# Performance work log

Hardware: AMD Instinct MI355X
Metric: run time of the kernel (lower is better)

Reference implementation:

```python
import jax, jax.numpy as jnp
import numpy as np
from jax import lax

EPS = 1e-5
D_STATE = 16
D_CONV = 4
DT_RANK = 4  # ceil(d_model/16) with d_model=64 (mamba_ssm default)


def _conv3d(x, w, pad, groups=1):
    return lax.conv_general_dilated(
        x, w, (1, 1, 1), pad,
        dimension_numbers=('NCDHW', 'OIDHW', 'NCDHW'),
        feature_group_count=groups)


def _inorm(x, g, b):
    # InstanceNorm3d: per-sample, per-channel stats over (Z,H,W), biased var, eps=1e-5
    m = x.mean(axis=(2, 3, 4), keepdims=True)
    v = x.var(axis=(2, 3, 4), keepdims=True)
    xn = (x - m) * lax.rsqrt(v + EPS)
    return xn * g[None, :, None, None, None] + b[None, :, None, None, None]


def _ln(x, g, b):
    m = x.mean(-1, keepdims=True)
    v = x.var(-1, keepdims=True)
    return (x - m) * lax.rsqrt(v + EPS) * g + b


def _forward(x, c1_w, in1_g, in1_b, c2_w, in2_g, in2_b,
             dw_w, pw_w, inr_g, inr_b,
             ln_g, ln_b,
             in_proj_w, conv1d_w, conv1d_b, x_proj_w,
             dt_proj_w, dt_proj_b, A_log, D_p, out_proj_w,
             proj_w, proj_b, pn_g, pn_b):
    B, _, Z, H, W = x.shape
    pad233 = [(1, 1), (1, 1), (1, 1)]  # kernel (2,3,3): Z grows by 1 each conv
    # ---- VolumeConvBlock ----
    h = _conv3d(x, c1_w, pad233)
    h = jax.nn.leaky_relu(_inorm(h, in1_g, in1_b), 0.01)
    h = _conv3d(h, c2_w, pad233)
    h = jax.nn.leaky_relu(_inorm(h, in2_g, in2_b), 0.01)
    h = h[:, :, :Z]  # out[:, :, :x.shape[2]]
    C = h.shape[1]
    # ---- ZMambaBlock ----
    residual = h
    # DepthwiseSpatialRefine
    pre = _conv3d(h, dw_w, [(0, 0), (1, 1), (1, 1)], groups=C)
    pre = _conv3d(pre, pw_w, [(0, 0), (0, 0), (0, 0)])
    pre = jax.nn.silu(_inorm(pre, inr_g, inr_b))
    x2 = h + pre
    # [B,C,Z,H,W] -> [B*H*W, Z, C]
    seq = jnp.transpose(x2, (0, 3, 4, 2, 1)).reshape(B * H * W, Z, C)
    seq = _ln(seq, ln_g, ln_b)
    # ---- Mamba ----
    di = in_proj_w.shape[0] // 2  # d_inner
    xz = seq @ in_proj_w.T  # [N, Z, 2*di]
    x_in, z = xz[..., :di], xz[..., di:]
    # causal depthwise conv1d along Z (pad left d_conv-1 == pad both then truncate)
    xc = lax.conv_general_dilated(
        jnp.transpose(x_in, (0, 2, 1)), conv1d_w, (1,), [(D_CONV - 1, 0)],
        dimension_numbers=('NCH', 'OIH', 'NCH'), feature_group_count=di)
    xc = xc + conv1d_b[None, :, None]
    xa = jax.nn.silu(jnp.transpose(xc, (0, 2, 1)))  # [N, Z, di]
    x_dbl = xa @ x_proj_w.T  # [N, Z, dt_rank + 2*d_state]
    dt = jax.nn.softplus(x_dbl[..., :DT_RANK] @ dt_proj_w.T + dt_proj_b)  # [N,Z,di]
    Bm = x_dbl[..., DT_RANK:DT_RANK + D_STATE]  # [N,Z,ds]
    Cm = x_dbl[..., DT_RANK + D_STATE:]         # [N,Z,ds]
    A = -jnp.exp(A_log)  # [di, ds]
    N = xa.shape[0]

    def step(hst, inp):
        dt_t, B_t, C_t, u_t = inp  # [N,di],[N,ds],[N,ds],[N,di]
        hst = jnp.exp(dt_t[:, :, None] * A) * hst + (dt_t * u_t)[:, :, None] * B_t[:, None, :]
        y_t = jnp.einsum('nds,ns->nd', hst, C_t)
        return hst, y_t

    h0 = jnp.zeros((N, di, D_STATE), dtype=xa.dtype)
    _, ys = lax.scan(step, h0,
                     (jnp.transpose(dt, (1, 0, 2)), jnp.transpose(Bm, (1, 0, 2)),
                      jnp.transpose(Cm, (1, 0, 2)), jnp.transpose(xa, (1, 0, 2))))
    y = jnp.transpose(ys, (1, 0, 2)) + D_p * xa  # [N,Z,di]
    y = y * jax.nn.silu(z)
    seq = y @ out_proj_w.T  # back to [N,Z,C]
    # proj linear
    seq = seq @ proj_w.T + proj_b
    # [B*H*W,Z,C] -> [B,C,Z,H,W]
    x3 = jnp.transpose(seq.reshape(B, H, W, Z, C), (0, 4, 3, 1, 2))
    x3 = _inorm(x3, pn_g, pn_b)
    return residual + x3


def setup_inputs() -> dict:
    key = jax.random.key(0)
    ks = jax.random.split(key, 20)
    IC, OC = 32, 64
    DI = 2 * OC  # d_inner = expand * d_model
    B, Z, H, W = 1, 32, 64, 64
    f32 = jnp.float32
    inp = {
        'x': jax.random.normal(ks[0], (B, IC, Z, H, W), f32),
        'c1_w': jax.random.normal(ks[1], (OC, IC, 2, 3, 3), f32) * 0.05,
        'in1_g': jnp.ones((OC,), f32), 'in1_b': jnp.zeros((OC,), f32),
        'c2_w': jax.random.normal(ks[2], (OC, OC, 2, 3, 3), f32) * 0.04,
        'in2_g': jnp.ones((OC,), f32), 'in2_b': jnp.zeros((OC,), f32),
        'dw_w': jax.random.normal(ks[3], (OC, 1, 1, 3, 3), f32) * 0.3,
        'pw_w': jax.random.normal(ks[4], (OC, OC, 1, 1, 1), f32) * 0.12,
        'inr_g': jnp.ones((OC,), f32), 'inr_b': jnp.zeros((OC,), f32),
        'ln_g': jnp.ones((OC,), f32), 'ln_b': jnp.zeros((OC,), f32),
        'in_proj_w': jax.random.normal(ks[5], (2 * DI, OC), f32) * 0.12,
        'conv1d_w': jax.random.normal(ks[6], (DI, 1, D_CONV), f32) * 0.4,
        'conv1d_b': jnp.zeros((DI,), f32),
        'x_proj_w': jax.random.normal(ks[7], (DT_RANK + 2 * D_STATE, DI), f32) * 0.08,
        'dt_proj_w': jax.random.normal(ks[8], (DI, DT_RANK), f32) * 0.4,
        'dt_proj_b': jax.random.uniform(ks[9], (DI,), f32, -4.0, -1.0),
        'A_log': jnp.log(jnp.tile(jnp.arange(1, D_STATE + 1, dtype=f32), (DI, 1))),
        'D_p': jnp.ones((DI,), f32),
        'out_proj_w': jax.random.normal(ks[10], (OC, DI), f32) * 0.08,
        'proj_w': jax.random.normal(ks[11], (OC, OC), f32) * 0.12,
        'proj_b': jnp.zeros((OC,), f32),
        'pn_g': jnp.ones((OC,), f32), 'pn_b': jnp.zeros((OC,), f32),
    }
    return inp


def reference(x, c1_w, in1_g, in1_b, c2_w, in2_g, in2_b,
              dw_w, pw_w, inr_g, inr_b, ln_g, ln_b,
              in_proj_w, conv1d_w, conv1d_b, x_proj_w,
              dt_proj_w, dt_proj_b, A_log, D_p, out_proj_w,
              proj_w, proj_b, pn_g, pn_b):
    return _forward(x, c1_w, in1_g, in1_b, c2_w, in2_g, in2_b,
                    dw_w, pw_w, inr_g, inr_b, ln_g, ln_b,
                    in_proj_w, conv1d_w, conv1d_b, x_proj_w,
                    dt_proj_w, dt_proj_b, A_log, D_p, out_proj_w,
                    proj_w, proj_b, pn_g, pn_b)
```

## Files before the change

kernel.cpp:

```cpp
#include <hip/hip_runtime.h>
#include <hip/hip_bf16.h>

#define NTHREADS 256

typedef __attribute__((ext_vector_type(8))) short bs8_t;
typedef __attribute__((ext_vector_type(4))) float f4_t;

__device__ __forceinline__ float bf2f(__hip_bfloat16 v) { return __bfloat162float(v); }
__device__ __forceinline__ __hip_bfloat16 f2bf(float v) { return __float2bfloat16(v); }
__device__ __forceinline__ float b2f_lo(unsigned int p) { return __uint_as_float(p << 16); }
__device__ __forceinline__ float b2f_hi(unsigned int p) { return __uint_as_float(p & 0xffff0000u); }
__device__ __forceinline__ float sigm(float x) { return 1.f / (1.f + __expf(-x)); }
__device__ __forceinline__ float leaky(float x) { return x > 0.f ? x : 0.01f * x; }
__device__ __forceinline__ float sane(float x) { return fminf(fmaxf(x, -1e9f), 1e9f); }
__device__ __forceinline__ unsigned packbf(float a, float b) {
  union { __hip_bfloat16 h[2]; unsigned u; } cv;
  cv.h[0] = f2bf(a); cv.h[1] = f2bf(b);
  return cv.u;
}
__device__ __forceinline__ float ldf(const void* p, long i, int f) {
  return f ? ((const float*)p)[i] : bf2f(((const __hip_bfloat16*)p)[i]);
}
__device__ __forceinline__ float exp2_fast(float x) {
  float r;
  asm("v_exp_f32 %0, %1" : "=v"(r) : "v"(x));
  return r;
}

__global__ void k_detect(const void* xp, int* flag) {
  __shared__ int cnt[NTHREADS];
  const __hip_bfloat16* h = (const __hip_bfloat16*)xp;
  int t = threadIdx.x;
  int c = 0;
  for (int j = 0; j < 8; j++) {
    float v = fabsf(bf2f(h[(t * 8 + j) * 2]));
    if (v > 1e-12f && v < 1e12f) c++;
  }
  cnt[t] = c;
  __syncthreads();
  for (int s = 128; s > 0; s >>= 1) {
    if (t < s) cnt[t] += cnt[t + s];
    __syncthreads();
  }
  if (t == 0) *flag = (cnt[0] > 1433) ? 0 : 1;
}

__global__ void k_prepcvt(const void* __restrict__ in, __hip_bfloat16* __restrict__ out,
                          int n, const int* __restrict__ flagp) {
  int f = *flagp;
  int gid = blockIdx.x * NTHREADS + threadIdx.x;
  if (gid < n) out[gid] = f2bf(ldf(in, gid, f));
}

__global__ __launch_bounds__(NTHREADS) void k_pad1(const void* __restrict__ x,
                                                   __hip_bfloat16* __restrict__ P1,
                                                   const int* __restrict__ flagp) {
  __shared__ float tile[64 * 33];
  int f = *flagp;
  int zp = blockIdx.x / 66, yp = blockIdx.x % 66;
  long rowbase = ((long)zp * 66 + yp) * 66 * 32;
  int t = threadIdx.x;
  if (zp == 0 || zp == 33 || yp == 0 || yp == 65) {
    for (int i = t; i < 2112; i += NTHREADS) P1[rowbase + i] = f2bf(0.f);
    return;
  }
  int z = zp - 1, y = yp - 1;
#pragma unroll
  for (int j = 0; j < 8; j++) {
    int idx = t + j * NTHREADS;
    int ci = idx >> 6, xx = idx & 63;
    tile[xx * 33 + ci] = ldf(x, (long)(ci * 32 + z) * 4096 + y * 64 + xx, f);
  }
  __syncthreads();
#pragma unroll
  for (int j = 0; j < 8; j++) {
    int idx = t + j * NTHREADS;
    int xx = idx >> 5, ci = idx & 31;
    P1[rowbase + (xx + 1) * 32 + ci] = f2bf(tile[xx * 33 + ci]);
  }
  if (t < 32) P1[rowbase + t] = f2bf(0.f);
  else if (t < 64) P1[rowbase + 65 * 32 + (t - 32)] = f2bf(0.f);
}

__global__ void k_prepw(const void* __restrict__ cw, __hip_bfloat16* __restrict__ W,
                        int CI, const int* __restrict__ flagp) {
  int f = *flagp;
  int gid = blockIdx.x * NTHREADS + threadIdx.x;
  int s = gid / (64 * CI);
  int rem = gid % (64 * CI);
  int co = rem / CI, ci = rem % CI;
  W[gid] = f2bf(ldf(cw, (long)(co * CI + ci) * 18 + s, f));
}

template <int CI, int CIP>
__global__ __launch_bounds__(NTHREADS) void k_gemm_conv(const __hip_bfloat16* __restrict__ Pb,
                                                        const __hip_bfloat16* __restrict__ Wb,
                                                        __hip_bfloat16* __restrict__ out,
                                                        float* __restrict__ gacc) {
  __shared__ unsigned short Wl[3 * 64 * CIP];
  __shared__ float sred[256], qred[256];
  const unsigned short* P = (const unsigned short*)Pb;
  const unsigned short* W = (const unsigned short*)Wb;
  int t = threadIdx.x;
  int wv = t >> 6, lane = t & 63;
  int m = lane & 15, quad = lane >> 4;
  int zo  = blockIdx.x >> 5;
  int rem = blockIdx.x & 31;
  int y   = ((rem >> 1) << 2) + wv;
  int xb  = (rem & 1) << 5;
  f4_t zero4 = {0.f, 0.f, 0.f, 0.f};
  f4_t acc[2][4];
#pragma unroll
  for (int mt = 0; mt < 2; mt++)
#pragma unroll
    for (int nt = 0; nt < 4; nt++) acc[mt][nt] = zero4;

  const int NV = 3 * 64 * CI / 8;
  for (int kz = 0; kz < 2; kz++) {
    for (int ky = 0; ky < 3; ky++) {
      __syncthreads();
      int s0 = (kz * 3 + ky) * 3;
      const uint4* wsrc4 = (const uint4*)(W + (long)s0 * 64 * CI);
      for (int i4 = t; i4 < NV; i4 += NTHREADS) {
        int idx = i4 * 8;
        int kx = idx / (64 * CI), rem2 = idx % (64 * CI);
        int co = rem2 / CI, g = (rem2 % CI) >> 3;
        *(uint4*)&Wl[(kx * 64 + co) * CIP + g * 8] = wsrc4[i4];
      }
      __syncthreads();
      int pz = zo + kz, py = y + ky;
      const unsigned short* prow = P + ((long)(pz * 66 + py) * 66) * CI;
#pragma unroll
      for (int kx = 0; kx < 3; kx++) {
#pragma unroll
        for (int ch = 0; ch < CI / 32; ch++) {
          int kof = kx * CI + ch * 32 + quad * 8;
          bs8_t a0 = *(const bs8_t*)(prow + (xb + 0 * 16 + m) * CI + kof);
          bs8_t a1 = *(const bs8_t*)(prow + (xb + 1 * 16 + m) * CI + kof);
#pragma unroll
          for (int nt = 0; nt < 4; nt++) {
            bs8_t b = *(const bs8_t*)&Wl[(kx * 64 + nt * 16 + m) * CIP + ch * 32 + quad * 8];
            acc[0][nt] = __builtin_amdgcn_mfma_f32_16x16x32_bf16(a0, b, acc[0][nt], 0, 0, 0);
            acc[1][nt] = __builtin_amdgcn_mfma_f32_16x16x32_bf16(a1, b, acc[1][nt], 0, 0, 0);
          }
        }
      }
    }
  }
  long obase = ((long)(zo * 64 + y) * 64) * 64;
  float psum[4], pq[4];
#pragma unroll
  for (int nt = 0; nt < 4; nt++) {
    int co = nt * 16 + m;
    float s = 0.f, q = 0.f;
#pragma unroll
    for (int mt = 0; mt < 2; mt++)
#pragma unroll
      for (int rg = 0; rg < 4; rg++) {
        float v = acc[mt][nt][rg];
        int xx = xb + mt * 16 + quad * 4 + rg;
        out[obase + xx * 64 + co] = f2bf(v);
        s += v;
        q += v * v;
      }
    psum[nt] = s;
    pq[nt] = q;
  }
#pragma unroll
  for (int nt = 0; nt < 4; nt++) {
    psum[nt] += __shfl_xor(psum[nt], 16, 64);
    psum[nt] += __shfl_xor(psum[nt], 32, 64);
    pq[nt]   += __shfl_xor(pq[nt], 16, 64);
    pq[nt]   += __shfl_xor(pq[nt], 32, 64);
  }
  if (quad == 0) {
#pragma unroll
    for (int nt = 0; nt < 4; nt++) {
      sred[wv * 64 + nt * 16 + m] = psum[nt];
      qred[wv * 64 + nt * 16 + m] = pq[nt];
    }
  }
  __syncthreads();
  if (t < 64) {
    atomicAdd(&gacc[t], sred[t] + sred[64 + t] + sred[128 + t] + sred[192 + t]);
    atomicAdd(&gacc[64 + t], qred[t] + qred[64 + t] + qred[128 + t] + qred[192 + t]);
  }
}

__global__ void k_finalize(const float* __restrict__ acc, const void* __restrict__ g,
                           const void* __restrict__ b, float* __restrict__ ss, float invN,
                           const int* __restrict__ flagp) {
  int f = *flagp;
  int t = threadIdx.x;
  float mean = acc[t] * invN;
  float var  = acc[64 + t] * invN - mean * mean;
  float rstd = rsqrtf(fmaxf(var, 0.f) + 1e-5f);
  float sc   = ldf(g, t, f) * rstd;
  ss[t]      = sc;
  ss[64 + t] = ldf(b, t, f) - mean * sc;
}

__global__ __launch_bounds__(NTHREADS) void k_normpad(const __hip_bfloat16* __restrict__ in,
                                                      const float* __restrict__ ss,
                                                      __hip_bfloat16* __restrict__ P2) {
  int zp = blockIdx.x / 66, yp = blockIdx.x % 66;
  long rowbase = ((long)zp * 66 + yp) * 66 * 64;
  int t = threadIdx.x;
  if (zp == 0 || zp == 34 || yp == 0 || yp == 65) {
    for (int i = t; i < 4224; i += NTHREADS) P2[rowbase + i] = f2bf(0.f);
    return;
  }
  int z = zp - 1, y = yp - 1;
#pragma unroll
  for (int j = 0; j < 16; j++) {
    int idx = t + j * NTHREADS;
    int xx = idx >> 6, co = idx & 63;
    float v = bf2f(in[((long)(z * 64 + y) * 64 + xx) * 64 + co]) * ss[co] + ss[64 + co];
    P2[rowbase + (xx + 1) * 64 + co] = f2bf(leaky(v));
  }
  if (t < 64) P2[rowbase + t] = f2bf(0.f);
  else if (t < 128) P2[rowbase + 65 * 64 + (t - 64)] = f2bf(0.f);
}

__global__ __launch_bounds__(NTHREADS) void k_hslice_cl(const __hip_bfloat16* __restrict__ in,
                                                        const float* __restrict__ ss,
                                                        __hip_bfloat16* __restrict__ hcl,
                                                        void* __restrict__ resid,
                                                        const int* __restrict__ flagp) {
  __shared__ float tile[64 * 65];
  int f = *flagp;
  int z = blockIdx.x >> 6, y = blockIdx.x & 63;
  long r0 = (long)z * 4096 + y * 64;
  int t = threadIdx.x;
#pragma unroll
  for (int j = 0; j < 16; j++) {
    int idx = t + j * NTHREADS;
    int xx = idx >> 6, co = idx & 63;
    float v = leaky(bf2f(in[(r0 + xx) * 64 + co]) * ss[co] + ss[64 + co]);
    hcl[(r0 + xx) * 64 + co] = f2bf(v);
    tile[xx * 65 + co] = v;
  }
  __syncthreads();
#pragma unroll
  for (int j = 0; j < 16; j++) {
    int idx = t + j * NTHREADS;
    int co = idx >> 6, xx = idx & 63;
    long off = (long)co * 131072 + r0 + xx;
    if (f) ((float*)resid)[off] = tile[xx * 65 + co];
    else   ((__hip_bfloat16*)resid)[off] = f2bf(tile[xx * 65 + co]);
  }
}

__global__ __launch_bounds__(NTHREADS) void k_dwpw_mfma(const __hip_bfloat16* __restrict__ hcl,
                                                        const void* __restrict__ dwb,
                                                        const __hip_bfloat16* __restrict__ pwbb,
                                                        __hip_bfloat16* __restrict__ out,
                                                        float* __restrict__ acc,
                                                        const int* __restrict__ flagp) {
  __shared__ unsigned short hl[3 * 64 * 64];
  __shared__ unsigned short dwt[64 * 72];
  __shared__ unsigned short pwl[64 * 72];
  __shared__ float dwl[576];
  __shared__ float sred[256], qred[256];
  int f = *flagp;
  int t = threadIdx.x;
  int z = blockIdx.x >> 6, y = blockIdx.x & 63;
  for (int i = t; i < 576; i += NTHREADS) dwl[i] = ldf(dwb, i, f);
  {
    const uint4* ps4 = (const uint4*)pwbb;
#pragma unroll
    for (int j = 0; j < 2; j++) {
      int i = t + j * NTHREADS;
      int row = i >> 3, g = i & 7;
      *(uint4*)&pwl[row * 72 + g * 8] = ps4[i];
    }
  }
  {
    const unsigned short* hsrc = (const unsigned short*)hcl;
    uint4* hl4 = (uint4*)hl;
#pragma unroll
    for (int j = 0; j < 6; j++) {
      int i = t + j * NTHREADS;
      int dy = i / 512, rem = i % 512;
      int ry = y - 1 + dy;
      uint4 v = make_uint4(0u, 0u, 0u, 0u);
      if ((unsigned)ry < 64u)
        v = *(const uint4*)(hsrc + ((long)z * 4096 + ry * 64) * 64 + rem * 8);
      hl4[i] = v;
    }
  }
  __syncthreads();
  const unsigned* hl32 = (const unsigned*)hl;
  unsigned* dwt32 = (unsigned*)dwt;
#pragma unroll
  for (int j = 0; j < 8; j++) {
    int idx = t + j * NTHREADS;
    int xx = idx >> 5, cp = idx & 31;
    float a0 = 0.f, a1 = 0.f;
#pragma unroll
    for (int dy = 0; dy < 3; dy++)
#pragma unroll
      for (int dx = 0; dx < 3; dx++) {
        int xv = xx - 1 + dx;
        if ((unsigned)xv < 64u) {
          unsigned hv = hl32[(dy * 64 + xv) * 32 + cp];
          a0 = fmaf(b2f_lo(hv), dwl[(cp * 2) * 9 + dy * 3 + dx], a0);
          a1 = fmaf(b2f_hi(hv), dwl[(cp * 2 + 1) * 9 + dy * 3 + dx], a1);
        }
      }
    dwt32[xx * 36 + cp] = packbf(a0, a1);
  }
  __syncthreads();
  int wv = t >> 6, lane = t & 63;
  int m = lane & 15, quad = lane >> 4;
  f4_t zero4 = {0.f, 0.f, 0.f, 0.f};
  f4_t acc4[4];
#pragma unroll
  for (int nt = 0; nt < 4; nt++) acc4[nt] = zero4;
#pragma unroll
  for (int ch = 0; ch < 2; ch++) {
    bs8_t a = *(const bs8_t*)&dwt[(wv * 16 + m) * 72 + ch * 32 + quad * 8];
#pragma unroll
    for (int nt = 0; nt < 4; nt++) {
      bs8_t b = *(const bs8_t*)&pwl[(nt * 16 + m) * 72 + ch * 32 + quad * 8];
      acc4[nt] = __builtin_amdgcn_mfma_f32_16x16x32_bf16(a, b, acc4[nt], 0, 0, 0);
    }
  }
  long obase = ((long)z * 4096 + y * 64) * 64;
  float psum[4], pq[4];
#pragma unroll
  for (int nt = 0; nt < 4; nt++) {
    float s = 0.f, q = 0.f;
#pragma unroll
    for (int rg = 0; rg < 4; rg++) {
      float v = acc4[nt][rg];
      int xx = wv * 16 + quad * 4 + rg;
      out[obase + xx * 64 + nt * 16 + m] = f2bf(v);
      s += v;
      q += v * v;
    }
    psum[nt] = s;
    pq[nt] = q;
  }
#pragma unroll
  for (int nt = 0; nt < 4; nt++) {
    psum[nt] += __shfl_xor(psum[nt], 16, 64);
    psum[nt] += __shfl_xor(psum[nt], 32, 64);
    pq[nt]   += __shfl_xor(pq[nt], 16, 64);
    pq[nt]   += __shfl_xor(pq[nt], 32, 64);
  }
  if (quad == 0) {
#pragma unroll
    for (int nt = 0; nt < 4; nt++) {
      sred[wv * 64 + nt * 16 + m] = psum[nt];
      qred[wv * 64 + nt * 16 + m] = pq[nt];
    }
  }
  __syncthreads();
  if (t < 64) {
    atomicAdd(&acc[t], sred[t] + sred[64 + t] + sred[128 + t] + sred[192 + t]);
    atomicAdd(&acc[64 + t], qred[t] + qred[64 + t] + qred[128 + t] + qred[192 + t]);
  }
}

__global__ __launch_bounds__(NTHREADS) void k_x2ln_cl(const __hip_bfloat16* __restrict__ hcl,
                                                      const __hip_bfloat16* __restrict__ p2,
                                                      const float* __restrict__ ssr,
                                                      const void* __restrict__ lng,
                                                      const void* __restrict__ lnb,
                                                      __hip_bfloat16* __restrict__ out,
                                                      const int* __restrict__ flagp) {
  __shared__ float sc[64], sh[64], sg[64], sb[64];
  int f = *flagp;
  int t = threadIdx.x;
  if (t < 64) {
    sc[t] = ssr[t];
    sh[t] = ssr[64 + t];
    sg[t] = ldf(lng, t, f);
    sb[t] = ldf(lnb, t, f);
  }
  __syncthreads();
  long r = (long)blockIdx.x * NTHREADS + t;
  const uint4* hp = (const uint4*)(hcl + r * 64);
  const uint4* pp = (const uint4*)(p2 + r * 64);
  float v[64];
  float s1 = 0.f;
#pragma unroll
  for (int q = 0; q < 8; q++) {
    uint4 hu = hp[q], pu = pp[q];
    float hv[8] = {b2f_lo(hu.x), b2f_hi(hu.x), b2f_lo(hu.y), b2f_hi(hu.y),
                   b2f_lo(hu.z), b2f_hi(hu.z), b2f_lo(hu.w), b2f_hi(hu.w)};
    float pv[8] = {b2f_lo(pu.x), b2f_hi(pu.x), b2f_lo(pu.y), b2f_hi(pu.y),
                   b2f_lo(pu.z), b2f_hi(pu.z), b2f_lo(pu.w), b2f_hi(pu.w)};
#pragma unroll
    for (int i = 0; i < 8; i++) {
      int c = q * 8 + i;
      float pn = sc[c] * pv[i] + sh[c];
      float x2 = hv[i] + pn * sigm(pn);
      v[c] = x2;
      s1 += x2;
    }
  }
  float m = s1 * (1.f / 64.f);
  float s2 = 0.f;
#pragma unroll
  for (int c = 0; c < 64; c++) {
    float d = v[c] - m;
    s2 += d * d;
  }
  float rstd = rsqrtf(s2 * (1.f / 64.f) + 1e-5f);
  uint4* o4 = (uint4*)(out + r * 64);
#pragma unroll
  for (int q = 0; q < 8; q++) {
    int c = q * 8;
    uint4 o;
    o.x = packbf((v[c + 0] - m) * rstd * sg[c + 0] + sb[c + 0],
                 (v[c + 1] - m) * rstd * sg[c + 1] + sb[c + 1]);
    o.y = packbf((v[c + 2] - m) * rstd * sg[c + 2] + sb[c + 2],
                 (v[c + 3] - m) * rstd * sg[c + 3] + sb[c + 3]);
    o.z = packbf((v[c + 4] - m) * rstd * sg[c + 4] + sb[c + 4],
                 (v[c + 5] - m) * rstd * sg[c + 5] + sb[c + 5]);
    o.w = packbf((v[c + 6] - m) * rstd * sg[c + 6] + sb[c + 6],
                 (v[c + 7] - m) * rstd * sg[c + 7] + sb[c + 7]);
    o4[q] = o;
  }
}

__global__ __launch_bounds__(NTHREADS) void k_inproj_mfma(const __hip_bfloat16* __restrict__ seq,
                                                          const __hip_bfloat16* __restrict__ Wbf,
                                                          __hip_bfloat16* __restrict__ x_in,
                                                          __hip_bfloat16* __restrict__ zg) {
  __shared__ unsigned short Wl[256 * 72];
  const uint4* ws4 = (const uint4*)Wbf;
  int t = threadIdx.x;
#pragma unroll
  for (int j = 0; j < 8; j++) {
    int i4 = t + j * NTHREADS;
    int row = i4 >> 3, g = i4 & 7;
    *(uint4*)&Wl[row * 72 + g * 8] = ws4[i4];
  }
  __syncthreads();
  int wv = t >> 6, lane = t & 63;
  int m = lane & 15, quad = lane >> 4;
  long m0 = (long)blockIdx.x * 64;
  int n0 = wv * 64;
  f4_t zero4 = {0.f, 0.f, 0.f, 0.f};
  f4_t acc[4][4];
#pragma unroll
  for (int mt = 0; mt < 4; mt++)
#pragma unroll
    for (int nt = 0; nt < 4; nt++) acc[mt][nt] = zero4;
  const unsigned short* sp = (const unsigned short*)seq;
#pragma unroll
  for (int ch = 0; ch < 2; ch++) {
    int kof = ch * 32 + quad * 8;
    bs8_t a0 = *(const bs8_t*)(sp + (m0 + 0 * 16 + m) * 64 + kof);
    bs8_t a1 = *(const bs8_t*)(sp + (m0 + 1 * 16 + m) * 64 + kof);
    bs8_t a2 = *(const bs8_t*)(sp + (m0 + 2 * 16 + m) * 64 + kof);
    bs8_t a3 = *(const bs8_t*)(sp + (m0 + 3 * 16 + m) * 64 + kof);
#pragma unroll
    for (int nt = 0; nt < 4; nt++) {
      bs8_t b = *(const bs8_t*)&Wl[(n0 + nt * 16 + m) * 72 + kof];
      acc[0][nt] = __builtin_amdgcn_mfma_f32_16x16x32_bf16(a0, b, acc[0][nt], 0, 0, 0);
      acc[1][nt] = __builtin_amdgcn_mfma_f32_16x16x32_bf16(a1, b, acc[1][nt], 0, 0, 0);
      acc[2][nt] = __builtin_amdgcn_mfma_f32_16x16x32_bf16(a2, b, acc[2][nt], 0, 0, 0);
      acc[3][nt] = __builtin_amdgcn_mfma_f32_16x16x32_bf16(a3, b, acc[3][nt], 0, 0, 0);
    }
  }
  __hip_bfloat16* obuf = (n0 < 128) ? x_in : zg;
  int cbase = (n0 < 128) ? n0 : (n0 - 128);
#pragma unroll
  for (int mt = 0; mt < 4; mt++)
#pragma unroll
    for (int nt = 0; nt < 4; nt++) {
      int col = cbase + nt * 16 + m;
#pragma unroll
      for (int rg = 0; rg < 4; rg++) {
        long row = m0 + mt * 16 + quad * 4 + rg;
        obuf[row * 128 + col] = f2bf(acc[mt][nt][rg]);
      }
    }
}

__global__ __launch_bounds__(NTHREADS) void k_conv1d_ip(__hip_bfloat16* xio,
                                                        const void* __restrict__ wb,
                                                        const void* __restrict__ bb,
                                                        const int* __restrict__ flagp) {
  int f = *flagp;
  int gid = blockIdx.x * NTHREADS + threadIdx.x;
  int d = gid & 127, nl = gid >> 7;
  float w0 = ldf(wb, d * 4 + 0, f), w1 = ldf(wb, d * 4 + 1, f);
  float w2 = ldf(wb, d * 4 + 2, f), w3 = ldf(wb, d * 4 + 3, f);
  float bias = ldf(bb, d, f);
  const size_t stride = 4096u * 128u;
  size_t off0 = (size_t)nl * 128 + d;
  float xv[32];
#pragma unroll
  for (int z = 0; z < 32; z++) xv[z] = bf2f(xio[off0 + (size_t)z * stride]);
  float h0 = 0.f, h1 = 0.f, h2 = 0.f;
#pragma unroll
  for (int z = 0; z < 32; z++) {
    float cur = xv[z];
    float a = bias;
    a = fmaf(h0, w0, a);
    a = fmaf(h1, w1, a);
    a = fmaf(h2, w2, a);
    a = fmaf(cur, w3, a);
    xv[z] = a * sigm(a);
    h0 = h1; h1 = h2; h2 = cur;
  }
#pragma unroll
  for (int z = 0; z < 32; z++) xio[off0 + (size_t)z * stride] = f2bf(xv[z]);
}

__global__ __launch_bounds__(NTHREADS) void k_xproj_mfma(const __hip_bfloat16* __restrict__ A,
                                                         const __hip_bfloat16* __restrict__ Wbf,
                                                         float* __restrict__ dtin,
                                                         float* __restrict__ BC) {
  __shared__ unsigned short Wl[48 * 136];
  const uint4* ws4 = (const uint4*)Wbf;
  int t = threadIdx.x;
#pragma unroll
  for (int j = 0; j < 3; j++) {
    int i4 = t + j * NTHREADS;
    int row = i4 >> 4, g = i4 & 15;
    uint4 v = make_uint4(0u, 0u, 0u, 0u);
    if (row < 36) v = ws4[row * 16 + g];
    *(uint4*)&Wl[row * 136 + g * 8] = v;
  }
  __syncthreads();
  int wv = t >> 6, lane = t & 63;
  int m = lane & 15, quad = lane >> 4;
  long m0 = (long)blockIdx.x * 256 + wv * 64;
  f4_t zero4 = {0.f, 0.f, 0.f, 0.f};
  f4_t acc[4][3];
#pragma unroll
  for (int mt = 0; mt < 4; mt++)
#pragma unroll
    for (int nt = 0; nt < 3; nt++) acc[mt][nt] = zero4;
  const unsigned short* ap = (const unsigned short*)A;
#pragma unroll
  for (int ch = 0; ch < 4; ch++) {
    int kof = ch * 32 + quad * 8;
    bs8_t a0 = *(const bs8_t*)(ap + (m0 + 0 * 16 + m) * 128 + kof);
    bs8_t a1 = *(const bs8_t*)(ap + (m0 + 1 * 16 + m) * 128 + kof);
    bs8_t a2 = *(const bs8_t*)(ap + (m0 + 2 * 16 + m) * 128 + kof);
    bs8_t a3 = *(const bs8_t*)(ap + (m0 + 3 * 16 + m) * 128 + kof);
#pragma unroll
    for (int nt = 0; nt < 3; nt++) {
      bs8_t b = *(const bs8_t*)&Wl[(nt * 16 + m) * 136 + kof];
      acc[0][nt] = __builtin_amdgcn_mfma_f32_16x16x32_bf16(a0, b, acc[0][nt], 0, 0, 0);
      acc[1][nt] = __builtin_amdgcn_mfma_f32_16x16x32_bf16(a1, b, acc[1][nt], 0, 0, 0);
      acc[2][nt] = __builtin_amdgcn_mfma_f32_16x16x32_bf16(a2, b, acc[2][nt], 0, 0, 0);
      acc[3][nt] = __builtin_amdgcn_mfma_f32_16x16x32_bf16(a3, b, acc[3][nt], 0, 0, 0);
    }
  }
#pragma unroll
  for (int mt = 0; mt < 4; mt++)
#pragma unroll
    for (int nt = 0; nt < 3; nt++) {
      int col = nt * 16 + m;
#pragma unroll
      for (int rg = 0; rg < 4; rg++) {
        long row = m0 + mt * 16 + quad * 4 + rg;
        float v = acc[mt][nt][rg];
        if (col < 4) dtin[row * 4 + col] = v;
        else if (col < 36) BC[row * 32 + (col - 4)] = v;
      }
    }
}

__global__ __launch_bounds__(NTHREADS) void k_scan(const float* __restrict__ dtin,
                                                   const float* __restrict__ BC,
                                                   __hip_bfloat16* __restrict__ uy,
                                                   const __hip_bfloat16* __restrict__ zg,
                                                   const void* __restrict__ dtw,
                                                   const void* __restrict__ dtb,
                                                   const void* __restrict__ Alog,
                                                   const void* __restrict__ Dp,
                                                   const int* __restrict__ flagp) {
  int f = *flagp;
  int gid = blockIdx.x * NTHREADS + threadIdx.x;
  int d = gid & 127, n = gid >> 7;
  float A2[16];
#pragma unroll
  for (int s = 0; s < 16; s++)
    A2[s] = -__expf(fminf(ldf(Alog, d * 16 + s, f), 60.f)) * 1.44269504088896f;
  float W0 = ldf(dtw, d * 4 + 0, f), W1 = ldf(dtw, d * 4 + 1, f);
  float W2 = ldf(dtw, d * 4 + 2, f), W3 = ldf(dtw, d * 4 + 3, f);
  float bias = ldf(dtb, d, f);
  float Dv = ldf(Dp, d, f);
  float a0 = A2[0];
  int geo = 1;
#pragma unroll
  for (int s = 1; s < 16; s++)
    geo &= (fabsf(A2[s] - (float)(s + 1) * a0) <= 1e-4f * fabsf(A2[s])) ? 1 : 0;
  geo = __all(geo);
  float st[16];
#pragma unroll
  for (int s = 0; s < 16; s++) st[s] = 0.f;
  if (geo) {
    int nu_ = __builtin_amdgcn_readfirstlane(n);
    const float4* bp0 = (const float4*)(BC + (size_t)nu_ * 32);
    const float4* dp0 = (const float4*)(dtin + (size_t)nu_ * 4);
    const __hip_bfloat16* up0 = uy + (size_t)n * 128 + d;
    const __hip_bfloat16* zp0 = zg + (size_t)n * 128 + d;
    __hip_bfloat16* uq = uy + (size_t)n * 128 + d;
    const size_t ustep = 4096u * 128u;
    float4 b0 = bp0[0], b1 = bp0[1], b2 = bp0[2], b3 = bp0[3];
    float4 c0 = bp0[4], c1 = bp0[5], c2 = bp0[6], c3 = bp0[7];
    float4 dt4 = dp0[0];
    float u  = sane(bf2f(*up0));
    float zv = sane(bf2f(*zp0));
#pragma unroll 2
    for (int z = 0; z < 32; z++) {
      int zn = (z < 31) ? z + 1 : 31;
      const float4* bpn = bp0 + (size_t)zn * 32768u;
      float4 nb0 = bpn[0], nb1 = bpn[1], nb2 = bpn[2], nb3 = bpn[3];
      float4 nc0 = bpn[4], nc1 = bpn[5], nc2 = bpn[6], nc3 = bpn[7];
      float4 ndt = dp0[(size_t)zn * 4096u];
      float nu  = sane(bf2f(up0[(size_t)zn * ustep]));
      float nzv = sane(bf2f(zp0[(size_t)zn * ustep]));
      float v = bias;
      v = fmaf(dt4.x, W0, v);
      v = fmaf(dt4.y, W1, v);
      v = fmaf(dt4.z, W2, v);
      v = fmaf(dt4.w, W3, v);
      float dtv = v > 20.f ? v : __logf(1.f + __expf(v));
      dtv = fminf(fmaxf(dtv, 0.f), 60.f);
      float du = dtv * u;
      float e1 = exp2_fast(dtv * a0);
      float e2 = e1 * e1;
      float es[16];
      es[0] = e1; es[1] = e2;
#pragma unroll
      for (int s = 2; s < 16; s++) es[s] = es[s - 2] * e2;
      float B[16] = {b0.x, b0.y, b0.z, b0.w, b1.x, b1.y, b1.z, b1.w,
                     b2.x, b2.y, b2.z, b2.w, b3.x, b3.y, b3.z, b3.w};
      float C[16] = {c0.x, c0.y, c0.z, c0.w, c1.x, c1.y, c1.z, c1.w,
                     c2.x, c2.y, c2.z, c2.w, c3.x, c3.y, c3.z, c3.w};
#pragma unroll
      for (int s = 0; s < 16; s++) st[s] = fmaf(es[s], st[s], du * B[s]);
      float y0 = 0.f, y1 = 0.f, y2 = 0.f, y3 = 0.f;
#pragma unroll
      for (int s = 0; s < 16; s += 4) {
        y0 = fmaf(st[s + 0], C[s + 0], y0);
        y1 = fmaf(st[s + 1], C[s + 1], y1);
        y2 = fmaf(st[s + 2], C[s + 2], y2);
        y3 = fmaf(st[s + 3], C[s + 3], y3);
      }
      float y = (y0 + y1) + (y2 + y3);
      y = sane((y + Dv * u) * (zv * sigm(zv)));
      uq[(size_t)z * ustep] = f2bf(y);
      b0 = nb0; b1 = nb1; b2 = nb2; b3 = nb3;
      c0 = nc0; c1 = nc1; c2 = nc2; c3 = nc3;
      dt4 = ndt; u = nu; zv = nzv;
    }
  } else {
#pragma unroll
    for (int s = 0; s < 16; s++) asm("" : "+v"(A2[s]));
    for (int z = 0; z < 32; z++) {
      size_t r = (size_t)z * 4096 + n;
      const float4* bp = (const float4*)(BC + r * 32);
      float4 dt4 = *(const float4*)(dtin + r * 4);
      float4 b0 = bp[0], b1 = bp[1], b2 = bp[2], b3 = bp[3];
      float4 c0 = bp[4], c1 = bp[5], c2 = bp[6], c3 = bp[7];
      float u = sane(bf2f(uy[r * 128 + d]));
      float zv = sane(bf2f(zg[r * 128 + d]));
      float v = bias;
      v = fmaf(dt4.x, W0, v);
      v = fmaf(dt4.y, W1, v);
      v = fmaf(dt4.z, W2, v);
      v = fmaf(dt4.w, W3, v);
      float dtv = v > 20.f ? v : __logf(1.f + __expf(v));
      dtv = fminf(fmaxf(dtv, 0.f), 60.f);
      float du = dtv * u;
      float B[16] = {b0.x, b0.y, b0.z, b0.w, b1.x, b1.y, b1.z, b1.w,
                     b2.x, b2.y, b2.z, b2.w, b3.x, b3.y, b3.z, b3.w};
      float C[16] = {c0.x, c0.y, c0.z, c0.w, c1.x, c1.y, c1.z, c1.w,
                     c2.x, c2.y, c2.z, c2.w, c3.x, c3.y, c3.z, c3.w};
      float y = 0.f;
#pragma unroll
      for (int s = 0; s < 16; s++) {
        float e = exp2_fast(dtv * A2[s]);
        st[s] = fmaf(e, st[s], du * B[s]);
        y = fmaf(st[s], C[s], y);
      }
      y = sane((y + Dv * u) * (zv * sigm(zv)));
      uy[r * 128 + d] = f2bf(y);
    }
  }
}

__global__ void k_wcomb(const void* __restrict__ pw, const void* __restrict__ opw,
                        __hip_bfloat16* __restrict__ wc, const int* __restrict__ flagp) {
  int f = *flagp;
  int gid = blockIdx.x * NTHREADS + threadIdx.x;
  int d = gid & 127, o = gid >> 7;
  float a = 0.f;
#pragma unroll
  for (int j = 0; j < 64; j++) a = fmaf(ldf(pw, o * 64 + j, f), ldf(opw, j * 128 + d, f), a);
  wc[(size_t)o * 128 + d] = f2bf(a);
}

__global__ __launch_bounds__(NTHREADS) void k_outproj_mfma(const __hip_bfloat16* __restrict__ A,
                                                           const __hip_bfloat16* __restrict__ Wcb,
                                                           const void* __restrict__ bias,
                                                           __hip_bfloat16* __restrict__ out,
                                                           float* __restrict__ gacc,
                                                           const int* __restrict__ flagp) {
  __shared__ unsigned short Wl[64 * 136];
  __shared__ float bl[64];
  __shared__ float sred[256], qred[256];
  int f = *flagp;
  int t = threadIdx.x;
  const uint4* ws4 = (const uint4*)Wcb;
#pragma unroll
  for (int j = 0; j < 4; j++) {
    int i4 = t + j * NTHREADS;
    int row = i4 >> 4, g = i4 & 15;
    *(uint4*)&Wl[row * 136 + g * 8] = ws4[i4];
  }
  if (t < 64) bl[t] = ldf(bias, t, f);
  __syncthreads();
  int wv = t >> 6, lane = t & 63;
  int m = lane & 15, quad = lane >> 4;
  long m0 = (long)blockIdx.x * 256 + wv * 64;
  f4_t zero4 = {0.f, 0.f, 0.f, 0.f};
  f4_t acc[4][4];
#pragma unroll
  for (int mt = 0; mt < 4; mt++)
#pragma unroll
    for (int nt = 0; nt < 4; nt++) acc[mt][nt] = zero4;
  const unsigned short* ap = (const unsigned short*)A;
#pragma unroll
  for (int ch = 0; ch < 4; ch++) {
    int kof = ch * 32 + quad * 8;
    bs8_t a0 = *(const bs8_t*)(ap + (m0 + 0 * 16 + m) * 128 + kof);
    bs8_t a1 = *(const bs8_t*)(ap + (m0 + 1 * 16 + m) * 128 + kof);
    bs8_t a2 = *(const bs8_t*)(ap + (m0 + 2 * 16 + m) * 128 + kof);
    bs8_t a3 = *(const bs8_t*)(ap + (m0 + 3 * 16 + m) * 128 + kof);
#pragma unroll
    for (int nt = 0; nt < 4; nt++) {
      bs8_t b = *(const bs8_t*)&Wl[(nt * 16 + m) * 136 + kof];
      acc[0][nt] = __builtin_amdgcn_mfma_f32_16x16x32_bf16(a0, b, acc[0][nt], 0, 0, 0);
      acc[1][nt] = __builtin_amdgcn_mfma_f32_16x16x32_bf16(a1, b, acc[1][nt], 0, 0, 0);
      acc[2][nt] = __builtin_amdgcn_mfma_f32_16x16x32_bf16(a2, b, acc[2][nt], 0, 0, 0);
      acc[3][nt] = __builtin_amdgcn_mfma_f32_16x16x32_bf16(a3, b, acc[3][nt], 0, 0, 0);
    }
  }
  float psum[4], pq[4];
#pragma unroll
  for (int nt = 0; nt < 4; nt++) {
    int co = nt * 16 + m;
    float s = 0.f, q = 0.f;
#pragma unroll
    for (int mt = 0; mt < 4; mt++)
#pragma unroll
      for (int rg = 0; rg < 4; rg++) {
        float v = sane(acc[mt][nt][rg] + bl[co]);
        long row = m0 + mt * 16 + quad * 4 + rg;
        out[row * 64 + co] = f2bf(v);
        s += v;
        q += v * v;
      }
    psum[nt] = s;
    pq[nt] = q;
  }
#pragma unroll
  for (int nt = 0; nt < 4; nt++) {
    psum[nt] += __shfl_xor(psum[nt], 16, 64);
    psum[nt] += __shfl_xor(psum[nt], 32, 64);
    pq[nt]   += __shfl_xor(pq[nt], 16, 64);
    pq[nt]   += __shfl_xor(pq[nt], 32, 64);
  }
  if (quad == 0) {
#pragma unroll
    for (int nt = 0; nt < 4; nt++) {
      sred[wv * 64 + nt * 16 + m] = psum[nt];
      qred[wv * 64 + nt * 16 + m] = pq[nt];
    }
  }
  __syncthreads();
  if (t < 64) {
    atomicAdd(&gacc[t], sred[t] + sred[64 + t] + sred[128 + t] + sred[192 + t]);
    atomicAdd(&gacc[64 + t], qred[t] + qred[64 + t] + qred[128 + t] + qred[192 + t]);
  }
}

__global__ __launch_bounds__(NTHREADS) void k_final(const __hip_bfloat16* __restrict__ s2,
                                                    void* __restrict__ io,
                                                    const float* __restrict__ ss,
                                                    const int* __restrict__ flagp) {
  __shared__ float tile[64 * 65];
  __shared__ float sc[64], sh[64];
  int f = *flagp;
  int t = threadIdx.x;
  if (t < 64) {
    sc[t] = ss[t];
    sh[t] = ss[64 + t];
  }
  int z = blockIdx.x >> 6, n0 = (blockIdx.x & 63) << 6;
  size_t base = ((size_t)z * 4096 + n0) * 64;
  __syncthreads();
#pragma unroll
  for (int jj = 0; jj < 16; jj++) {
    int id = t + jj * NTHREADS;
    int i = id >> 6, c = id & 63;
    float v = sane(bf2f(s2[base + id]));
    tile[i * 65 + c] = sc[c] * v + sh[c];
  }
  __syncthreads();
#pragma unroll
  for (int jj = 0; jj < 16; jj++) {
    int id = t + jj * NTHREADS;
    int c = id >> 6, nl = id & 63;
    size_t off = (size_t)c * 131072 + (size_t)z * 4096 + n0 + nl;
    if (f) {
      float* o = (float*)io;
      o[off] = sane(o[off] + tile[nl * 65 + c]);
    } else {
      __hip_bfloat16* o = (__hip_bfloat16*)io;
      o[off] = f2bf(sane(bf2f(o[off]) + tile[nl * 65 + c]));
    }
  }
}

extern "C" void kernel_launch(void* const* d_in, const int* in_sizes, int n_in,
                              void* d_out, int out_size, void* d_ws, size_t ws_size,
                              hipStream_t stream) {
  (void)in_sizes; (void)n_in; (void)out_size; (void)ws_size;
  const void* x        = d_in[0];
  const void* c1_w     = d_in[1];
  const void* in1_g    = d_in[2];
  const void* in1_b    = d_in[3];
  const void* c2_w     = d_in[4];
  const void* in2_g    = d_in[5];
  const void* in2_b    = d_in[6];
  const void* dw_w     = d_in[7];
  const void* pw_w     = d_in[8];
  const void* inr_g    = d_in[9];
  const void* inr_b    = d_in[10];
  const void* ln_g     = d_in[11];
  const void* ln_b     = d_in[12];
  const void* in_proj_w= d_in[13];
  const void* conv1d_w = d_in[14];
  const void* conv1d_b = d_in[15];
  const void* x_proj_w = d_in[16];
  const void* dt_proj_w= d_in[17];
  const void* dt_proj_b= d_in[18];
  const void* A_log    = d_in[19];
  const void* D_p      = d_in[20];
  const void* out_proj_w=d_in[21];
  const void* proj_w   = d_in[22];
  const void* proj_b   = d_in[23];
  const void* pn_g     = d_in[24];
  const void* pn_b     = d_in[25];

  char* wb = (char*)d_ws;
  __hip_bfloat16* P1   = (__hip_bfloat16*)wb;
  __hip_bfloat16* P2   = (__hip_bfloat16*)wb;
  __hip_bfloat16* zgb  = (__hip_bfloat16*)wb;
  __hip_bfloat16* s2   = (__hip_bfloat16*)wb;
  __hip_bfloat16* c1raw = (__hip_bfloat16*)(wb + 33554432);
  __hip_bfloat16* c2raw = (__hip_bfloat16*)(wb + 33554432);
  __hip_bfloat16* pre2  = (__hip_bfloat16*)(wb + 33554432);
  __hip_bfloat16* x_in  = (__hip_bfloat16*)(wb + 33554432);
  __hip_bfloat16* hcl   = (__hip_bfloat16*)(wb + 51380224);
  __hip_bfloat16* seq   = (__hip_bfloat16*)(wb + 68157440);
  float*          BCf   = (float*)(wb + 68157440);
  __hip_bfloat16* W1b   = (__hip_bfloat16*)(wb + 84934656);
  __hip_bfloat16* W2b   = (__hip_bfloat16*)(wb + 85008384);
  __hip_bfloat16* inwb  = (__hip_bfloat16*)(wb + 85155840);
  __hip_bfloat16* wcombb= (__hip_bfloat16*)(wb + 85188608);
  __hip_bfloat16* pwbb  = (__hip_bfloat16*)(wb + 85204992);
  __hip_bfloat16* xpwb  = (__hip_bfloat16*)(wb + 85213184);
  float*          fst   = (float*)(wb + 85222400);
  float*          dtinf = (float*)(wb + 85229568);

  float* acc_in1 = fst;
  float* acc_in2 = fst + 128;
  float* acc_inr = fst + 256;
  float* acc_pn  = fst + 384;
  float* ss_in1  = fst + 512;
  float* ss_in2  = fst + 640;
  float* ss_inr  = fst + 768;
  float* ss_pn   = fst + 896;
  int*   flagp   = (int*)(fst + 1024);

  hipMemsetAsync(fst, 0, 512 * sizeof(float), stream);

  k_detect<<<1, NTHREADS, 0, stream>>>(x, flagp);
  k_pad1<<<34 * 66, NTHREADS, 0, stream>>>(x, P1, flagp);
  k_prepw<<<144, NTHREADS, 0, stream>>>(c1_w, W1b, 32, flagp);
  k_prepw<<<288, NTHREADS, 0, stream>>>(c2_w, W2b, 64, flagp);
  k_prepcvt<<<64, NTHREADS, 0, stream>>>(in_proj_w, inwb, 16384, flagp);
  k_prepcvt<<<16, NTHREADS, 0, stream>>>(pw_w, pwbb, 4096, flagp);
  k_prepcvt<<<18, NTHREADS, 0, stream>>>(x_proj_w, xpwb, 4608, flagp);
  k_wcomb<<<32, NTHREADS, 0, stream>>>(proj_w, out_proj_w, wcombb, flagp);

  k_gemm_conv<32, 40><<<33 * 32, NTHREADS, 0, stream>>>(P1, W1b, c1raw, acc_in1);
  k_finalize<<<1, 64, 0, stream>>>(acc_in1, in1_g, in1_b, ss_in1, 1.0f / 135168.0f, flagp);
  k_normpad<<<35 * 66, NTHREADS, 0, stream>>>(c1raw, ss_in1, P2);

  k_gemm_conv<64, 88><<<34 * 32, NTHREADS, 0, stream>>>(P2, W2b, c2raw, acc_in2);
  k_finalize<<<1, 64, 0, stream>>>(acc_in2, in2_g, in2_b, ss_in2, 1.0f / 139264.0f, flagp);
  k_hslice_cl<<<2048, NTHREADS, 0, stream>>>(c2raw, ss_in2, hcl, d_out, flagp);

  k_dwpw_mfma<<<2048, NTHREADS, 0, stream>>>(hcl, dw_w, pwbb, pre2, acc_inr, flagp);
  k_finalize<<<1, 64, 0, stream>>>(acc_inr, inr_g, inr_b, ss_inr, 1.0f / 131072.0f, flagp);
  k_x2ln_cl<<<512, NTHREADS, 0, stream>>>(hcl, pre2, ss_inr, ln_g, ln_b, seq, flagp);

  k_inproj_mfma<<<2048, NTHREADS, 0, stream>>>(seq, inwb, x_in, zgb);
  k_conv1d_ip<<<2048, NTHREADS, 0, stream>>>(x_in, conv1d_w, conv1d_b, flagp);
  k_xproj_mfma<<<512, NTHREADS, 0, stream>>>(x_in, xpwb, dtinf, BCf);
  k_scan<<<2048, NTHREADS, 0, stream>>>(dtinf, BCf, x_in, zgb, dt_proj_w, dt_proj_b, A_log, D_p, flagp);
  k_outproj_mfma<<<512, NTHREADS, 0, stream>>>(x_in, wcombb, proj_b, s2, acc_pn, flagp);

  k_finalize<<<1, 64, 0, stream>>>(acc_pn, pn_g, pn_b, ss_pn, 1.0f / 131072.0f, flagp);
  k_final<<<2048, NTHREADS, 0, stream>>>(s2, d_out, ss_pn, flagp);
}
```

Measured before the change: 516.0 us.

## Stage a full kz slice of conv weights in LDS with XOR swizzle

The implicit-GEMM 3D conv kernel now loads all nine (ky,kx) weight taps for each kz into shared memory at once, instead of three taps per ky iteration. This cuts the barrier and reload count from six to two per block. Row padding is replaced by an XOR swizzle of 8-element groups to avoid LDS bank conflicts. LDS use grows (to 72KB for CI=64), which may lower occupancy per CU.

```diff
diff --git a/kernel.cpp b/kernel.cpp
--- a/kernel.cpp
+++ b/kernel.cpp
@@ -92,15 +92,15 @@
   W[gid] = f2bf(ldf(cw, (long)(co * CI + ci) * 18 + s, f));
 }
 
-template <int CI, int CIP>
+template <int CI>
 __global__ __launch_bounds__(NTHREADS) void k_gemm_conv(const __hip_bfloat16* __restrict__ Pb,
                                                         const __hip_bfloat16* __restrict__ Wb,
                                                         __hip_bfloat16* __restrict__ out,
                                                         float* __restrict__ gacc) {
-  __shared__ unsigned short Wl[3 * 64 * CIP];
+  constexpr int G = CI / 8;
+  __shared__ unsigned short Wl[9 * 64 * CI];
   __shared__ float sred[256], qred[256];
   const unsigned short* P = (const unsigned short*)Pb;
-  const unsigned short* W = (const unsigned short*)Wb;
   int t = threadIdx.x;
   int wv = t >> 6, lane = t & 63;
   int m = lane & 15, quad = lane >> 4;
@@ -115,20 +115,20 @@
 #pragma unroll
     for (int nt = 0; nt < 4; nt++) acc[mt][nt] = zero4;
 
-  const int NV = 3 * 64 * CI / 8;
+  const int NV = 9 * 64 * G;
   for (int kz = 0; kz < 2; kz++) {
+    __syncthreads();
+    const uint4* wsrc4 = (const uint4*)(const void*)Wb + (long)kz * NV;
+    for (int i4 = t; i4 < NV; i4 += NTHREADS) {
+      int r = i4 / G, g = i4 & (G - 1);
+      int gs = g ^ (r & (G - 1));
+      *(uint4*)&Wl[r * CI + gs * 8] = wsrc4[i4];
+    }
+    __syncthreads();
+    int pz = zo + kz;
+#pragma unroll
     for (int ky = 0; ky < 3; ky++) {
-      __syncthreads();
-      int s0 = (kz * 3 + ky) * 3;
-      const uint4* wsrc4 = (const uint4*)(W + (long)s0 * 64 * CI);
-      for (int i4 = t; i4 < NV; i4 += NTHREADS) {
-        int idx = i4 * 8;
-        int kx = idx / (64 * CI), rem2 = idx % (64 * CI);
-        int co = rem2 / CI, g = (rem2 % CI) >> 3;
-        *(uint4*)&Wl[(kx * 64 + co) * CIP + g * 8] = wsrc4[i4];
-      }
-      __syncthreads();
-      int pz = zo + kz, py = y + ky;
+      int py = y + ky;
       const unsigned short* prow = P + ((long)(pz * 66 + py) * 66) * CI;
 #pragma unroll
       for (int kx = 0; kx < 3; kx++) {
@@ -137,9 +137,12 @@
           int kof = kx * CI + ch * 32 + quad * 8;
           bs8_t a0 = *(const bs8_t*)(prow + (xb + 0 * 16 + m) * CI + kof);
           bs8_t a1 = *(const bs8_t*)(prow + (xb + 1 * 16 + m) * CI + kof);
+          int g = ch * 4 + quad;
 #pragma unroll
           for (int nt = 0; nt < 4; nt++) {
-            bs8_t b = *(const bs8_t*)&Wl[(kx * 64 + nt * 16 + m) * CIP + ch * 32 + quad * 8];
+            int row = (ky * 3 + kx) * 64 + nt * 16 + m;
+            int gs = g ^ (row & (G - 1));
+            bs8_t b = *(const bs8_t*)&Wl[row * CI + gs * 8];
             acc[0][nt] = __builtin_amdgcn_mfma_f32_16x16x32_bf16(a0, b, acc[0][nt], 0, 0, 0);
             acc[1][nt] = __builtin_amdgcn_mfma_f32_16x16x32_bf16(a1, b, acc[1][nt], 0, 0, 0);
           }
@@ -899,11 +902,11 @@
   k_prepcvt<<<18, NTHREADS, 0, stream>>>(x_proj_w, xpwb, 4608, flagp);
   k_wcomb<<<32, NTHREADS, 0, stream>>>(proj_w, out_proj_w, wcombb, flagp);
 
-  k_gemm_conv<32, 40><<<33 * 32, NTHREADS, 0, stream>>>(P1, W1b, c1raw, acc_in1);
+  k_gemm_conv<32><<<33 * 32, NTHREADS, 0, stream>>>(P1, W1b, c1raw, acc_in1);
   k_finalize<<<1, 64, 0, stream>>>(acc_in1, in1_g, in1_b, ss_in1, 1.0f / 135168.0f, flagp);
   k_normpad<<<35 * 66, NTHREADS, 0, stream>>>(c1raw, ss_in1, P2);
 
-  k_gemm_conv<64, 88><<<34 * 32, NTHREADS, 0, stream>>>(P2, W2b, c2raw, acc_in2);
+  k_gemm_conv<64><<<34 * 32, NTHREADS, 0, stream>>>(P2, W2b, c2raw, acc_in2);
   k_finalize<<<1, 64, 0, stream>>>(acc_in2, in2_g, in2_b, ss_in2, 1.0f / 139264.0f, flagp);
   k_hslice_cl<<<2048, NTHREADS, 0, stream>>>(c2raw, ss_in2, hcl, d_out, flagp);
 
```

Result: slower. 533.6 us (+3.4%).
